# Performance work log

Measured on AMD Instinct MI355X. Metric: run time of the kernel, lower is better.

The kernel has to match this reference:

```python
import jax, jax.numpy as jnp
import numpy as np
import math

W = 256      # attention_window
DIL = 1      # attention_dilation
H = 12       # num heads
HD = 64      # head dim
E = 768      # hidden size


def setup_inputs() -> dict:
    key = jax.random.key(0)
    ks = jax.random.split(key, 4)
    B, S = 2, 4096
    s = 0.02
    inp = {"hidden_states": jax.random.normal(ks[0], (B, S, E), jnp.float32)}
    inp["Wq"] = jax.random.normal(ks[1], (E, E), jnp.float32) * s
    inp["Wk"] = jax.random.normal(ks[2], (E, E), jnp.float32) * s
    inp["Wv"] = jax.random.normal(ks[3], (E, E), jnp.float32) * s
    inp["bq"] = jnp.zeros((E,), jnp.float32)
    inp["bk"] = jnp.zeros((E,), jnp.float32)
    inp["bv"] = jnp.zeros((E,), jnp.float32)
    return inp


def _banded_attention(q, k, v):
    # q,k,v: [B,S,H,HD]; banded attention with window W, dilation DIL
    B, S, Hh, D = q.shape
    offsets = (jnp.arange(2 * W + 1) - W) * DIL  # relative key offsets
    pos = jnp.arange(S)

    def score(off):
        idx = pos + off
        valid = (idx >= 0) & (idx < S)          # mask_invalid_locations
        kk = k[:, jnp.clip(idx, 0, S - 1)]      # [B,S,H,HD] shifted keys
        s = jnp.einsum('bshd,bshd->bsh', q, kk)
        return jnp.where(valid[None, :, None], s, -jnp.inf)

    # diagonaled_mm(q, k): [2W+1, B, S, H] -> [B, S, H, 2W+1]
    scores = jax.lax.map(score, offsets)
    probs = jax.nn.softmax(jnp.moveaxis(scores, 0, -1), axis=-1)

    # diagonaled_mm(probs, v, is_t1_diagonaled=True): accumulate over band
    def step(acc, j):
        off = offsets[j]
        idx = pos + off
        valid = (idx >= 0) & (idx < S)
        vv = v[:, jnp.clip(idx, 0, S - 1)]
        p = jnp.where(valid[None, :, None], probs[..., j], 0.0)
        return acc + p[..., None] * vv, None

    out, _ = jax.lax.scan(step, jnp.zeros_like(v), jnp.arange(2 * W + 1))
    return out


def reference(hidden_states, Wq, bq, Wk, bk, Wv, bv):
    B, S, _ = hidden_states.shape
    q = (hidden_states @ Wq.T + bq) / math.sqrt(HD)
    k = hidden_states @ Wk.T + bk
    v = hidden_states @ Wv.T + bv
    q = q.reshape(B, S, H, HD)
    k = k.reshape(B, S, H, HD)
    v = v.reshape(B, S, H, HD)
    out = _banded_attention(q, k, v)  # [B,S,H,HD]
    return out.reshape(B, S, E)
```

## Files before the change

kernel.cpp:

```cpp
#include <hip/hip_runtime.h>

#define S_LEN 4096
#define BATCH 2
#define EMB   768
#define NH    12
#define HDIM  64
#define WIN   256

using f32x4  = __attribute__((ext_vector_type(4))) float;
using bf16x8 = __attribute__((ext_vector_type(8))) short;
using u16x4  = __attribute__((ext_vector_type(4))) unsigned short;
using u16x8  = __attribute__((ext_vector_type(8))) unsigned short;

#define AS1 __attribute__((address_space(1)))
#define AS3 __attribute__((address_space(3)))

__device__ __forceinline__ unsigned short f2bf(float x) {
    unsigned int u = __float_as_uint(x);
    return (unsigned short)((u + 0x7fffu + ((u >> 16) & 1u)) >> 16);
}
__device__ __forceinline__ unsigned short f2bf_fast(float x) {
    return (unsigned short)((__float_as_uint(x) + 0x8000u) >> 16);
}

__global__ void cvt_all_kernel(const float* __restrict__ hs, const float* __restrict__ w0,
                               const float* __restrict__ w1, const float* __restrict__ w2,
                               unsigned short* __restrict__ ohs, unsigned short* __restrict__ o0,
                               unsigned short* __restrict__ o1, unsigned short* __restrict__ o2) {
    int blk = blockIdx.x;
    const float* in;
    unsigned short* out;
    int i;
    if (blk < 3072) { in = hs; out = ohs; i = blk * 256 + threadIdx.x; if (i >= 786432) return; }
    else {
        int wsel = (blk - 3072) / 288;
        int wblk = (blk - 3072) % 288;
        in  = (wsel == 0) ? w0 : (wsel == 1) ? w1 : w2;
        out = (wsel == 0) ? o0 : (wsel == 1) ? o1 : o2;
        i = wblk * 256 + threadIdx.x;
        if (i >= 73728) return;
    }
    const float4* p = reinterpret_cast<const float4*>(in) + (size_t)i * 2;
    float4 a = p[0];
    float4 b = p[1];
    u16x8 o;
    o[0] = f2bf(a.x); o[1] = f2bf(a.y); o[2] = f2bf(a.z); o[3] = f2bf(a.w);
    o[4] = f2bf(b.x); o[5] = f2bf(b.y); o[6] = f2bf(b.z); o[7] = f2bf(b.w);
    reinterpret_cast<u16x8*>(out)[i] = o;
}

#define NKT (EMB / 32)

__global__ __launch_bounds__(256) void qkv_gemm(
    const unsigned short* __restrict__ A,
    const unsigned short* __restrict__ Wq,
    const unsigned short* __restrict__ Wk,
    const unsigned short* __restrict__ Wv,
    const float* __restrict__ bq,
    const float* __restrict__ bk,
    const float* __restrict__ bv,
    unsigned short* __restrict__ qo,
    unsigned short* __restrict__ ko,
    unsigned short* __restrict__ vo)
{
    __shared__ unsigned short As[2][128 * 32];
    __shared__ unsigned short Bs[2][128 * 32];

    const int tid  = threadIdx.x;
    const int lane = tid & 63;
    const int wave = tid >> 6;

    const int mblk = blockIdx.x;
    const int nblk = blockIdx.y;
    const int wsel = nblk / 6;
    const int nloc0 = (nblk % 6) * 128;
    const unsigned short* Wp = (wsel == 0) ? Wq : ((wsel == 1) ? Wk : Wv);
    const int wm = wave >> 1, wn = wave & 1;

    f32x4 acc[4][4];
#pragma unroll
    for (int i = 0; i < 4; ++i)
#pragma unroll
        for (int j = 0; j < 4; ++j)
            acc[i][j] = (f32x4){0.f, 0.f, 0.f, 0.f};

    const int frow = lane & 15;
    const int g    = lane >> 4;

    const char* Abase = (const char*)(A  + (size_t)(mblk * 128) * EMB);
    const char* Bbase = (const char*)(Wp + (size_t)nloc0 * EMB);

    const int srow = tid >> 2;
    const int pb   = tid & 3;
    const int sblk = pb ^ ((srow >> 1) & 3);

#define GLDS(gp, lp) __builtin_amdgcn_global_load_lds((const AS1 unsigned int*)(gp), (AS3 unsigned int*)(lp), 16, 0, 0)
#define STG(q, t) do {                                                                                   \
    GLDS(Abase + (size_t)srow * 1536 + (t) * 64 + sblk * 16,        &As[q][srow * 32 + pb * 8]);         \
    GLDS(Abase + (size_t)(64 + srow) * 1536 + (t) * 64 + sblk * 16, &As[q][(64 + srow) * 32 + pb * 8]);  \
    GLDS(Bbase + (size_t)srow * 1536 + (t) * 64 + sblk * 16,        &Bs[q][srow * 32 + pb * 8]);         \
    GLDS(Bbase + (size_t)(64 + srow) * 1536 + (t) * 64 + sblk * 16, &Bs[q][(64 + srow) * 32 + pb * 8]);  \
} while (0)

    auto rdA = [&](int q, int mi) -> bf16x8 {
        int r = wm * 64 + mi * 16 + frow;
        return *reinterpret_cast<const bf16x8*>(&As[q][r * 32 + (g ^ ((r >> 1) & 3)) * 8]);
    };
    auto rdB = [&](int q, int ni) -> bf16x8 {
        int r = wn * 64 + ni * 16 + frow;
        return *reinterpret_cast<const bf16x8*>(&Bs[q][r * 32 + (g ^ ((r >> 1) & 3)) * 8]);
    };

#define KLOOP(SW) do {                                                                        \
    STG(0, 0);                                                                                \
    asm volatile("s_waitcnt vmcnt(0)" ::: "memory");                                          \
    __syncthreads();                                                                          \
    int cur = 0;                                                                              \
    _Pragma("unroll 1")                                                                       \
    for (int t = 0; t < NKT; ++t) {                                                           \
        if (t + 1 < NKT) STG(cur ^ 1, t + 1);                                                 \
        bf16x8 afr[4], bfr[4];                                                                \
        _Pragma("unroll") for (int ni = 0; ni < 4; ++ni) bfr[ni] = rdB(cur, ni);              \
        _Pragma("unroll") for (int mi = 0; mi < 4; ++mi) afr[mi] = rdA(cur, mi);              \
        __builtin_amdgcn_s_setprio(1);                                                        \
        _Pragma("unroll") for (int mi = 0; mi < 4; ++mi)                                      \
            _Pragma("unroll") for (int ni = 0; ni < 4; ++ni)                                  \
                acc[mi][ni] = (SW)                                                            \
                    ? __builtin_amdgcn_mfma_f32_16x16x32_bf16(bfr[ni], afr[mi], acc[mi][ni], 0, 0, 0)  \
                    : __builtin_amdgcn_mfma_f32_16x16x32_bf16(afr[mi], bfr[ni], acc[mi][ni], 0, 0, 0); \
        __builtin_amdgcn_s_setprio(0);                                                        \
        if (t + 1 < NKT) {                                                                    \
            asm volatile("s_waitcnt vmcnt(0)" ::: "memory");                                  \
            __syncthreads();                                                                  \
            cur ^= 1;                                                                         \
        }                                                                                     \
    }                                                                                         \
} while (0)

    if (wsel < 2) {
        KLOOP(1);
        const float* bias = (wsel == 0) ? bq : bk;
        unsigned short* op = (wsel == 0) ? qo : ko;
        const float qs = (wsel == 0) ? 0.125f : 1.0f;
#pragma unroll
        for (int mi = 0; mi < 4; ++mi) {
            int m = mblk * 128 + wm * 64 + mi * 16 + frow;
            int b = m >> 12, s = m & 4095;
#pragma unroll
            for (int ni = 0; ni < 4; ++ni) {
                int n0 = nloc0 + wn * 64 + ni * 16 + g * 4;
                float4 bb = *reinterpret_cast<const float4*>(&bias[n0]);
                int h = n0 >> 6, hd0 = n0 & 63;
                u16x4 pk;
                pk[0] = f2bf((acc[mi][ni][0] + bb.x) * qs);
                pk[1] = f2bf((acc[mi][ni][1] + bb.y) * qs);
                pk[2] = f2bf((acc[mi][ni][2] + bb.z) * qs);
                pk[3] = f2bf((acc[mi][ni][3] + bb.w) * qs);
                *reinterpret_cast<u16x4*>(&op[((size_t)(b * NH + h) * S_LEN + s) * HDIM + hd0]) = pk;
            }
        }
    } else {
        KLOOP(0);
#pragma unroll
        for (int mi = 0; mi < 4; ++mi) {
            int m0 = mblk * 128 + wm * 64 + mi * 16 + g * 4;
            int b = m0 >> 12, s0 = m0 & 4095;
#pragma unroll
            for (int ni = 0; ni < 4; ++ni) {
                int n = nloc0 + wn * 64 + ni * 16 + frow;
                float bb = bv[n];
                int h = n >> 6, hd = n & 63;
                u16x4 pk;
                pk[0] = f2bf(acc[mi][ni][0] + bb);
                pk[1] = f2bf(acc[mi][ni][1] + bb);
                pk[2] = f2bf(acc[mi][ni][2] + bb);
                pk[3] = f2bf(acc[mi][ni][3] + bb);
                *reinterpret_cast<u16x4*>(&vo[((size_t)(b * NH + h) * HDIM + hd) * S_LEN + s0]) = pk;
            }
        }
    }
}

#define QB   128
#define KC   64
#define NCHQ ((QB + 2 * WIN) / KC)

#define STAGE_ATT(buf, ks) do {                                                              \
    const unsigned short* kr_ = kp + (size_t)((ks) + srow) * HDIM + gblk * 8;                \
    __builtin_amdgcn_global_load_lds(                                                        \
        (const AS1 unsigned int*)kr_,                                                        \
        (AS3 unsigned int*)&Ksm[buf][wave * 512], 16, 0, 0);                                 \
    const unsigned short* vr_ = vp + (size_t)srow * S_LEN + (ks) + gblk * 8;                 \
    __builtin_amdgcn_global_load_lds(                                                        \
        (const AS1 unsigned int*)vr_,                                                        \
        (AS3 unsigned int*)&Vsm[buf][wave * 512], 16, 0, 0);                                 \
} while (0)

__global__ __launch_bounds__(512) void banded_attn(
    const unsigned short* __restrict__ qg,
    const unsigned short* __restrict__ kg,
    const unsigned short* __restrict__ vtg,
    float* __restrict__ out)
{
    __shared__ unsigned short Ksm[2][KC * HDIM];
    __shared__ unsigned short Vsm[2][HDIM * KC];
    __shared__ unsigned short Psm[8][16 * KC];

    const int tid  = threadIdx.x;
    const int wave = tid >> 6, lane = tid & 63;
    const int qb = blockIdx.x * QB;
    const int h  = blockIdx.y, b = blockIdx.z;

    const unsigned short* qp = qg  + (size_t)(b * NH + h) * S_LEN * HDIM;
    const unsigned short* kp = kg  + (size_t)(b * NH + h) * S_LEN * HDIM;
    const unsigned short* vp = vtg + (size_t)(b * NH + h) * HDIM * S_LEN;

    const int frow = lane & 15;
    const int g    = lane >> 4;
    const int fcol = g * 8;

    const int srow = tid >> 3;
    const int gblk = (tid & 7) ^ (srow & 7);

    bf16x8 qf[2];
    {
        const unsigned short* qr = qp + (size_t)(qb + wave * 16 + frow) * HDIM;
        qf[0] = *reinterpret_cast<const bf16x8*>(qr + fcol);
        qf[1] = *reinterpret_cast<const bf16x8*>(qr + 32 + fcol);
    }

    float l_part[4];
    f32x4 o_acc[4];
#pragma unroll
    for (int r = 0; r < 4; ++r) l_part[r] = 0.f;
#pragma unroll
    for (int ni = 0; ni < 4; ++ni) o_acc[ni] = (f32x4){0.f, 0.f, 0.f, 0.f};

    const int c_start = (qb < WIN) ? ((WIN - qb) >> 6) : 0;
    const int c_end   = min(NCHQ, (S_LEN + WIN - qb) >> 6);
    const int qw    = qb + wave * 16;
    const int qrow0 = qw + g * 4;

    const int w_lo = qw - WIN;
    const int w_hi = qw + 15 + WIN;

    int kb[4];
#pragma unroll
    for (int ni = 0; ni < 4; ++ni) kb[ni] = ni * 16 + frow;
    unsigned short* prow_p[4];
    int swz_r[4];
#pragma unroll
    for (int r = 0; r < 4; ++r) {
        int prow = g * 4 + r;
        prow_p[r] = &Psm[wave][prow * KC];
        swz_r[r]  = (prow & 7) << 3;
    }

    STAGE_ATT(0, qb - WIN + c_start * KC);
    asm volatile("s_waitcnt vmcnt(0)" ::: "memory");
    __syncthreads();

    int cur = 0;
    for (int c = c_start; c < c_end; ++c) {
        const int ks = qb - WIN + c * KC;
        if (c + 1 < c_end) STAGE_ATT(cur ^ 1, ks + KC);

        const bool active = (ks + KC - 1 >= w_lo) && (ks <= w_hi);
        if (active) {
            f32x4 sc[4];
#pragma unroll
            for (int ni = 0; ni < 4; ++ni) sc[ni] = (f32x4){0.f, 0.f, 0.f, 0.f};
#pragma unroll
            for (int ni = 0; ni < 4; ++ni) {
                int krow = ni * 16 + frow;
                int sw   = (krow & 7) << 3;
                bf16x8 kf0 = *reinterpret_cast<const bf16x8*>(&Ksm[cur][krow * KC + (fcol ^ sw)]);
                bf16x8 kf1 = *reinterpret_cast<const bf16x8*>(&Ksm[cur][krow * KC + ((32 + fcol) ^ sw)]);
                sc[ni] = __builtin_amdgcn_mfma_f32_16x16x32_bf16(qf[0], kf0, sc[ni], 0, 0, 0);
                sc[ni] = __builtin_amdgcn_mfma_f32_16x16x32_bf16(qf[1], kf1, sc[ni], 0, 0, 0);
            }

            const bool full = (ks >= qw - 241) && (ks <= qw + 193);
            float pm[4][4];
            if (full) {
#pragma unroll
                for (int ni = 0; ni < 4; ++ni)
#pragma unroll
                    for (int r = 0; r < 4; ++r)
                        pm[ni][r] = __expf(sc[ni][r]);
            } else {
#pragma unroll
                for (int ni = 0; ni < 4; ++ni) {
                    int d0 = qrow0 - (ks + kb[ni]);
#pragma unroll
                    for (int r = 0; r < 4; ++r) {
                        bool valid = (unsigned)(d0 + r + WIN) <= (unsigned)(2 * WIN);
                        pm[ni][r] = valid ? __expf(sc[ni][r]) : 0.f;
                    }
                }
            }
#pragma unroll
            for (int r = 0; r < 4; ++r) {
                l_part[r] += (pm[0][r] + pm[1][r]) + (pm[2][r] + pm[3][r]);
#pragma unroll
                for (int ni = 0; ni < 4; ++ni)
                    prow_p[r][kb[ni] ^ swz_r[r]] = f2bf_fast(pm[ni][r]);
            }

            asm volatile("s_waitcnt lgkmcnt(0)" ::: "memory");
            __builtin_amdgcn_sched_barrier(0);

            bf16x8 pf[2];
#pragma unroll
            for (int kk = 0; kk < 2; ++kk) {
                int sw = (frow & 7) << 3;
                pf[kk] = *reinterpret_cast<const bf16x8*>(&Psm[wave][frow * KC + ((kk * 32 + fcol) ^ sw)]);
            }
#pragma unroll
            for (int ni = 0; ni < 4; ++ni) {
                int vrow = ni * 16 + frow;
                int sw   = (vrow & 7) << 3;
#pragma unroll
                for (int kk = 0; kk < 2; ++kk) {
                    bf16x8 vf = *reinterpret_cast<const bf16x8*>(&Vsm[cur][vrow * KC + ((kk * 32 + fcol) ^ sw)]);
                    o_acc[ni] = __builtin_amdgcn_mfma_f32_16x16x32_bf16(pf[kk], vf, o_acc[ni], 0, 0, 0);
                }
            }
        }

        asm volatile("s_waitcnt vmcnt(0)" ::: "memory");
        __syncthreads();
        cur ^= 1;
    }

#pragma unroll
    for (int d = 1; d < 16; d <<= 1)
#pragma unroll
        for (int r = 0; r < 4; ++r)
            l_part[r] += __shfl_xor(l_part[r], d, 64);

#pragma unroll
    for (int r = 0; r < 4; ++r) {
        float inv = 1.0f / l_part[r];
        int s = qrow0 + r;
        size_t obase = ((size_t)b * S_LEN + s) * EMB + h * HDIM;
#pragma unroll
        for (int ni = 0; ni < 4; ++ni)
            out[obase + ni * 16 + frow] = o_acc[ni][r] * inv;
    }
}

extern "C" void kernel_launch(void* const* d_in, const int* in_sizes, int n_in,
                              void* d_out, int out_size, void* d_ws, size_t ws_size,
                              hipStream_t stream) {
    const float* hs = (const float*)d_in[0];
    const float* Wq = (const float*)d_in[1];
    const float* Wk = (const float*)d_in[2];
    const float* Wv = (const float*)d_in[3];
    const float* bq = (const float*)d_in[4];
    const float* bk = (const float*)d_in[5];
    const float* bv = (const float*)d_in[6];
    float* out = (float*)d_out;

    char* w = (char*)d_ws;
    unsigned short* hs_bf = (unsigned short*)w;
    unsigned short* wq_bf = (unsigned short*)(w + 12582912);
    unsigned short* wk_bf = wq_bf + 589824;
    unsigned short* wv_bf = wk_bf + 589824;
    unsigned short* q_ws  = (unsigned short*)(w + 12582912 + 3 * 1179648);
    unsigned short* k_ws  = q_ws + 6291456;
    unsigned short* v_ws  = k_ws + 6291456;

    cvt_all_kernel<<<3936, 256, 0, stream>>>(hs, Wq, Wk, Wv, hs_bf, wq_bf, wk_bf, wv_bf);

    qkv_gemm<<<dim3(64, 18), 256, 0, stream>>>(hs_bf, wq_bf, wk_bf, wv_bf,
                                               bq, bk, bv, q_ws, k_ws, v_ws);

    banded_attn<<<dim3(S_LEN / QB, NH, BATCH), 512, 0, stream>>>(q_ws, k_ws, v_ws, out);
}
```

Before: 93.83 us.

## Give each attention wave 32 query rows to reuse K/V fragments

The banded attention block shrinks from 8 waves of 16 query rows to 4 waves of 32 query rows. Each wave now reuses every K and V fragment read from LDS for two MFMA query sub-tiles, and the staging macro issues two loads per thread to fill the same tiles with half the threads. This halves LDS fragment reads per MFMA and the number of waves doing redundant band checks. In exchange each wave holds more registers and there are fewer waves per block to hide latency, and each wave's 32-row window covers more inactive or partially masked chunks.

After: 101.0 us. +7.7%, slower.

```diff
diff --git a/kernel.cpp b/kernel.cpp
--- a/kernel.cpp
+++ b/kernel.cpp
@@ -186,17 +186,21 @@
 #define NCHQ ((QB + 2 * WIN) / KC)
 
 #define STAGE_ATT(buf, ks) do {                                                              \
-    const unsigned short* kr_ = kp + (size_t)((ks) + srow) * HDIM + gblk * 8;                \
     __builtin_amdgcn_global_load_lds(                                                        \
-        (const AS1 unsigned int*)kr_,                                                        \
+        (const AS1 unsigned int*)(kp + (size_t)((ks) + srow) * HDIM + gblk * 8),             \
         (AS3 unsigned int*)&Ksm[buf][wave * 512], 16, 0, 0);                                 \
-    const unsigned short* vr_ = vp + (size_t)srow * S_LEN + (ks) + gblk * 8;                 \
     __builtin_amdgcn_global_load_lds(                                                        \
-        (const AS1 unsigned int*)vr_,                                                        \
+        (const AS1 unsigned int*)(kp + (size_t)((ks) + 32 + srow) * HDIM + gblk * 8),        \
+        (AS3 unsigned int*)&Ksm[buf][2048 + wave * 512], 16, 0, 0);                          \
+    __builtin_amdgcn_global_load_lds(                                                        \
+        (const AS1 unsigned int*)(vp + (size_t)srow * S_LEN + (ks) + gblk * 8),              \
         (AS3 unsigned int*)&Vsm[buf][wave * 512], 16, 0, 0);                                 \
+    __builtin_amdgcn_global_load_lds(                                                        \
+        (const AS1 unsigned int*)(vp + (size_t)(32 + srow) * S_LEN + (ks) + gblk * 8),       \
+        (AS3 unsigned int*)&Vsm[buf][2048 + wave * 512], 16, 0, 0);                          \
 } while (0)
 
-__global__ __launch_bounds__(512) void banded_attn(
+__global__ __launch_bounds__(256) void banded_attn(
     const unsigned short* __restrict__ qg,
     const unsigned short* __restrict__ kg,
     const unsigned short* __restrict__ vtg,
@@ -204,7 +208,7 @@
 {
     __shared__ unsigned short Ksm[2][KC * HDIM];
     __shared__ unsigned short Vsm[2][HDIM * KC];
-    __shared__ unsigned short Psm[8][16 * KC];
+    __shared__ unsigned short Psm[4][32 * KC];
 
     const int tid  = threadIdx.x;
     const int wave = tid >> 6, lane = tid & 63;
@@ -222,39 +226,32 @@
     const int srow = tid >> 3;
     const int gblk = (tid & 7) ^ (srow & 7);
 
-    bf16x8 qf[2];
-    {
-        const unsigned short* qr = qp + (size_t)(qb + wave * 16 + frow) * HDIM;
-        qf[0] = *reinterpret_cast<const bf16x8*>(qr + fcol);
-        qf[1] = *reinterpret_cast<const bf16x8*>(qr + 32 + fcol);
+    const int qw = qb + wave * 32;
+
+    bf16x8 qf[2][2];
+#pragma unroll
+    for (int qs = 0; qs < 2; ++qs) {
+        const unsigned short* qr = qp + (size_t)(qw + qs * 16 + frow) * HDIM;
+        qf[qs][0] = *reinterpret_cast<const bf16x8*>(qr + fcol);
+        qf[qs][1] = *reinterpret_cast<const bf16x8*>(qr + 32 + fcol);
     }
 
-    float l_part[4];
-    f32x4 o_acc[4];
-#pragma unroll
-    for (int r = 0; r < 4; ++r) l_part[r] = 0.f;
-#pragma unroll
-    for (int ni = 0; ni < 4; ++ni) o_acc[ni] = (f32x4){0.f, 0.f, 0.f, 0.f};
+    float l_part[2][4];
+    f32x4 o_acc[2][4];
+#pragma unroll
+    for (int qs = 0; qs < 2; ++qs)
+#pragma unroll
+        for (int r = 0; r < 4; ++r) l_part[qs][r] = 0.f;
+#pragma unroll
+    for (int qs = 0; qs < 2; ++qs)
+#pragma unroll
+        for (int ni = 0; ni < 4; ++ni) o_acc[qs][ni] = (f32x4){0.f, 0.f, 0.f, 0.f};
 
     const int c_start = (qb < WIN) ? ((WIN - qb) >> 6) : 0;
     const int c_end   = min(NCHQ, (S_LEN + WIN - qb) >> 6);
-    const int qw    = qb + wave * 16;
-    const int qrow0 = qw + g * 4;
 
     const int w_lo = qw - WIN;
-    const int w_hi = qw + 15 + WIN;
-
-    int kb[4];
-#pragma unroll
-    for (int ni = 0; ni < 4; ++ni) kb[ni] = ni * 16 + frow;
-    unsigned short* prow_p[4];
-    int swz_r[4];
-#pragma unroll
-    for (int r = 0; r < 4; ++r) {
-        int prow = g * 4 + r;
-        prow_p[r] = &Psm[wave][prow * KC];
-        swz_r[r]  = (prow & 7) << 3;
-    }
+    const int w_hi = qw + 31 + WIN;
 
     STAGE_ATT(0, qb - WIN + c_start * KC);
     asm volatile("s_waitcnt vmcnt(0)" ::: "memory");
@@ -267,54 +264,72 @@
 
         const bool active = (ks + KC - 1 >= w_lo) && (ks <= w_hi);
         if (active) {
-            f32x4 sc[4];
-#pragma unroll
-            for (int ni = 0; ni < 4; ++ni) sc[ni] = (f32x4){0.f, 0.f, 0.f, 0.f};
+            f32x4 sc[2][4];
+#pragma unroll
+            for (int qs = 0; qs < 2; ++qs)
+#pragma unroll
+                for (int ni = 0; ni < 4; ++ni) sc[qs][ni] = (f32x4){0.f, 0.f, 0.f, 0.f};
 #pragma unroll
             for (int ni = 0; ni < 4; ++ni) {
                 int krow = ni * 16 + frow;
                 int sw   = (krow & 7) << 3;
                 bf16x8 kf0 = *reinterpret_cast<const bf16x8*>(&Ksm[cur][krow * KC + (fcol ^ sw)]);
                 bf16x8 kf1 = *reinterpret_cast<const bf16x8*>(&Ksm[cur][krow * KC + ((32 + fcol) ^ sw)]);
-                sc[ni] = __builtin_amdgcn_mfma_f32_16x16x32_bf16(qf[0], kf0, sc[ni], 0, 0, 0);
-                sc[ni] = __builtin_amdgcn_mfma_f32_16x16x32_bf16(qf[1], kf1, sc[ni], 0, 0, 0);
-            }
-
-            const bool full = (ks >= qw - 241) && (ks <= qw + 193);
-            float pm[4][4];
+#pragma unroll
+                for (int qs = 0; qs < 2; ++qs) {
+                    sc[qs][ni] = __builtin_amdgcn_mfma_f32_16x16x32_bf16(qf[qs][0], kf0, sc[qs][ni], 0, 0, 0);
+                    sc[qs][ni] = __builtin_amdgcn_mfma_f32_16x16x32_bf16(qf[qs][1], kf1, sc[qs][ni], 0, 0, 0);
+                }
+            }
+
+            const bool full = (ks >= qw - 225) && (ks <= qw + 193);
+            float pm[2][4][4];
             if (full) {
 #pragma unroll
-                for (int ni = 0; ni < 4; ++ni)
-#pragma unroll
-                    for (int r = 0; r < 4; ++r)
-                        pm[ni][r] = __expf(sc[ni][r]);
+                for (int qs = 0; qs < 2; ++qs)
+#pragma unroll
+                    for (int ni = 0; ni < 4; ++ni)
+#pragma unroll
+                        for (int r = 0; r < 4; ++r)
+                            pm[qs][ni][r] = __expf(sc[qs][ni][r]);
             } else {
 #pragma unroll
-                for (int ni = 0; ni < 4; ++ni) {
-                    int d0 = qrow0 - (ks + kb[ni]);
-#pragma unroll
-                    for (int r = 0; r < 4; ++r) {
-                        bool valid = (unsigned)(d0 + r + WIN) <= (unsigned)(2 * WIN);
-                        pm[ni][r] = valid ? __expf(sc[ni][r]) : 0.f;
+                for (int qs = 0; qs < 2; ++qs) {
+                    int qrow0s = qw + qs * 16 + g * 4;
+#pragma unroll
+                    for (int ni = 0; ni < 4; ++ni) {
+                        int d0 = qrow0s - (ks + ni * 16 + frow);
+#pragma unroll
+                        for (int r = 0; r < 4; ++r) {
+                            bool valid = (unsigned)(d0 + r + WIN) <= (unsigned)(2 * WIN);
+                            pm[qs][ni][r] = valid ? __expf(sc[qs][ni][r]) : 0.f;
+                        }
                     }
                 }
             }
 #pragma unroll
-            for (int r = 0; r < 4; ++r) {
-                l_part[r] += (pm[0][r] + pm[1][r]) + (pm[2][r] + pm[3][r]);
-#pragma unroll
-                for (int ni = 0; ni < 4; ++ni)
-                    prow_p[r][kb[ni] ^ swz_r[r]] = f2bf_fast(pm[ni][r]);
-            }
+            for (int qs = 0; qs < 2; ++qs)
+#pragma unroll
+                for (int r = 0; r < 4; ++r) {
+                    l_part[qs][r] += (pm[qs][0][r] + pm[qs][1][r]) + (pm[qs][2][r] + pm[qs][3][r]);
+                    int prow = qs * 16 + g * 4 + r;
+                    int swz  = ((g * 4 + r) & 7) << 3;
+#pragma unroll
+                    for (int ni = 0; ni < 4; ++ni)
+                        Psm[wave][prow * KC + ((ni * 16 + frow) ^ swz)] = f2bf_fast(pm[qs][ni][r]);
+                }
 
             asm volatile("s_waitcnt lgkmcnt(0)" ::: "memory");
             __builtin_amdgcn_sched_barrier(0);
 
-            bf16x8 pf[2];
-#pragma unroll
-            for (int kk = 0; kk < 2; ++kk) {
+            bf16x8 pf[2][2];
+#pragma unroll
+            for (int qs = 0; qs < 2; ++qs) {
                 int sw = (frow & 7) << 3;
-                pf[kk] = *reinterpret_cast<const bf16x8*>(&Psm[wave][frow * KC + ((kk * 32 + fcol) ^ sw)]);
+#pragma unroll
+                for (int kk = 0; kk < 2; ++kk)
+                    pf[qs][kk] = *reinterpret_cast<const bf16x8*>(
+                        &Psm[wave][(qs * 16 + frow) * KC + ((kk * 32 + fcol) ^ sw)]);
             }
 #pragma unroll
             for (int ni = 0; ni < 4; ++ni) {
@@ -323,7 +338,9 @@
 #pragma unroll
                 for (int kk = 0; kk < 2; ++kk) {
                     bf16x8 vf = *reinterpret_cast<const bf16x8*>(&Vsm[cur][vrow * KC + ((kk * 32 + fcol) ^ sw)]);
-                    o_acc[ni] = __builtin_amdgcn_mfma_f32_16x16x32_bf16(pf[kk], vf, o_acc[ni], 0, 0, 0);
+#pragma unroll
+                    for (int qs = 0; qs < 2; ++qs)
+                        o_acc[qs][ni] = __builtin_amdgcn_mfma_f32_16x16x32_bf16(pf[qs][kk], vf, o_acc[qs][ni], 0, 0, 0);
                 }
             }
         }
@@ -336,17 +353,23 @@
 #pragma unroll
     for (int d = 1; d < 16; d <<= 1)
 #pragma unroll
-        for (int r = 0; r < 4; ++r)
-            l_part[r] += __shfl_xor(l_part[r], d, 64);
-
-#pragma unroll
-    for (int r = 0; r < 4; ++r) {
-        float inv = 1.0f / l_part[r];
-        int s = qrow0 + r;
-        size_t obase = ((size_t)b * S_LEN + s) * EMB + h * HDIM;
-#pragma unroll
-        for (int ni = 0; ni < 4; ++ni)
-            out[obase + ni * 16 + frow] = o_acc[ni][r] * inv;
+        for (int qs = 0; qs < 2; ++qs)
+#pragma unroll
+            for (int r = 0; r < 4; ++r)
+                l_part[qs][r] += __shfl_xor(l_part[qs][r], d, 64);
+
+#pragma unroll
+    for (int qs = 0; qs < 2; ++qs) {
+        int qrow0s = qw + qs * 16 + g * 4;
+#pragma unroll
+        for (int r = 0; r < 4; ++r) {
+            float inv = 1.0f / l_part[qs][r];
+            int s = qrow0s + r;
+            size_t obase = ((size_t)b * S_LEN + s) * EMB + h * HDIM;
+#pragma unroll
+            for (int ni = 0; ni < 4; ++ni)
+                out[obase + ni * 16 + frow] = o_acc[qs][ni][r] * inv;
+        }
     }
 }
 
@@ -376,5 +399,5 @@
     qkv_gemm<<<dim3(64, 18), 256, 0, stream>>>(hs_bf, wq_bf, wk_bf, wv_bf,
                                                bq, bk, bv, q_ws, k_ws, v_ws);
 
-    banded_attn<<<dim3(S_LEN / QB, NH, BATCH), 512, 0, stream>>>(q_ws, k_ws, v_ws, out);
-}
+    banded_attn<<<dim3(S_LEN / QB, NH, BATCH), 256, 0, stream>>>(q_ws, k_ws, v_ws, out);
+}
```
